# Performance work log

Hardware: AMD Instinct MI355X
Metric: run time of the kernel (lower is better)

## Reference

```python
import jax, jax.numpy as jnp
import numpy as np

D_MODEL = 1024
NUM_HEADS = 16
HEAD_DIM = D_MODEL // NUM_HEADS
B, S = 2, 2048


def setup_inputs() -> dict:
    key = jax.random.key(0)
    ks = jax.random.split(key, 8)
    scale = 1.0 / np.sqrt(D_MODEL)
    inp = {
        "query": jax.random.normal(ks[0], (B, S, D_MODEL), jnp.float32),
        "key": jax.random.normal(ks[1], (B, S, D_MODEL), jnp.float32),
        "value": jax.random.normal(ks[2], (B, S, D_MODEL), jnp.float32),
        # causal mask, broadcastable over batch and heads
        "mask": jnp.tril(jnp.ones((S, S), dtype=bool))[None, None, :, :],
        # torch nn.Linear weights: y = x @ W.T (+ b)
        "Wq": jax.random.normal(ks[3], (D_MODEL, D_MODEL), jnp.float32) * scale,
        "Wk": jax.random.normal(ks[4], (D_MODEL, D_MODEL), jnp.float32) * scale,
        "Wv": jax.random.normal(ks[5], (D_MODEL, D_MODEL), jnp.float32) * scale,
        "Wo": jax.random.normal(ks[6], (D_MODEL, D_MODEL), jnp.float32) * scale,
        "bo": jax.random.normal(ks[7], (D_MODEL,), jnp.float32) * scale,
    }
    return inp


def _split_heads(x):
    b, s, _ = x.shape
    return x.reshape(b, s, NUM_HEADS, HEAD_DIM).transpose(0, 2, 1, 3)  # [B,H,S,Dh]


def reference(query, key, value, mask, Wq, Wk, Wv, Wo, bo):
    q = _split_heads(query @ Wq.T)
    k = _split_heads(key @ Wk.T)
    v = _split_heads(value @ Wv.T)
    scores = jnp.einsum("bhqd,bhkd->bhqk", q, k) / jnp.sqrt(jnp.float32(HEAD_DIM))
    scores = jnp.where(mask, scores, jnp.float32(-jnp.inf))
    attn = jax.nn.softmax(scores, axis=-1)
    out = jnp.einsum("bhqk,bhkd->bhqd", attn, v)  # [B,H,S,Dh]
    out = out.transpose(0, 2, 1, 3).reshape(query.shape[0], q.shape[2], D_MODEL)
    return out @ Wo.T + bo
```

## Files before the change

kernel.cpp:

```cpp
#include <hip/hip_runtime.h>
#include <hip/hip_bf16.h>

#define DM   1024
#define NH   16
#define HD   64
#define SEQ  2048
#define BATCH 2
#define MTOT (BATCH*SEQ)

typedef unsigned short u16;
typedef __attribute__((ext_vector_type(8))) short bf16x8;
typedef __attribute__((ext_vector_type(4))) float f32x4;

__device__ __forceinline__ float bf2f(u16 h) {
  union { unsigned int i; float f; } u; u.i = ((unsigned int)h) << 16; return u.f;
}
__device__ __forceinline__ u16 f2bf(float f) {
  union { float f; unsigned int i; } u; u.f = f;
  unsigned int r = u.i + 0x7fffu + ((u.i >> 16) & 1u);
  return (u16)(r >> 16);
}

__global__ void detect_dtype(const u16* __restrict__ q, int* __restrict__ flag) {
  const int lane = threadIdx.x & 63;
  int cnt = 0;
  for (int i = 0; i < 8; i++) {
    int e = (q[i*64 + lane] >> 7) & 0xFF;
    unsigned long long m = __ballot(e >= 0x6E && e <= 0x8F);
    cnt += __popcll(m);
  }
  if (lane == 0) *flag = (cnt >= 400) ? 1 : 0;
}

__device__ __forceinline__ uint4 load8_bf16(const void* base, size_t elemOff, bool isf32) {
  if (!isf32) return *(const uint4*)((const u16*)base + elemOff);
  const float* f = (const float*)base + elemOff;
  f32x4 a = *(const f32x4*)f;
  f32x4 b = *(const f32x4*)(f + 4);
  union { u16 h[8]; uint4 v; } r;
  r.h[0]=f2bf(a[0]); r.h[1]=f2bf(a[1]); r.h[2]=f2bf(a[2]); r.h[3]=f2bf(a[3]);
  r.h[4]=f2bf(b[0]); r.h[5]=f2bf(b[1]); r.h[6]=f2bf(b[2]); r.h[7]=f2bf(b[3]);
  return r.v;
}

__global__ __launch_bounds__(256) void prep(
    const void* __restrict__ q, const void* __restrict__ k, const void* __restrict__ v,
    const void* __restrict__ wq, const void* __restrict__ wk, const void* __restrict__ wv,
    const void* __restrict__ wo, const void* __restrict__ bo,
    u16* __restrict__ Xq, u16* __restrict__ Xk, u16* __restrict__ Xv,
    u16* __restrict__ Wqb, u16* __restrict__ Wkb, u16* __restrict__ Wvb, u16* __restrict__ Wob,
    float* __restrict__ biasf, const int* __restrict__ dflag)
{
  const bool isf32 = (*dflag == 0);
  const int z = blockIdx.z;
  if (z == 7) {
    if (blockIdx.x == 0) {
      for (int i = threadIdx.x; i < DM; i += 256)
        biasf[i] = isf32 ? ((const float*)bo)[i] : bf2f(((const u16*)bo)[i]);
    }
    return;
  }
  const void* src; u16* dst; size_t n;
  switch (z) {
    case 0: src=q;  dst=Xq;  n=(size_t)MTOT*DM; break;
    case 1: src=k;  dst=Xk;  n=(size_t)MTOT*DM; break;
    case 2: src=v;  dst=Xv;  n=(size_t)MTOT*DM; break;
    case 3: src=wq; dst=Wqb; n=(size_t)DM*DM;   break;
    case 4: src=wk; dst=Wkb; n=(size_t)DM*DM;   break;
    case 5: src=wv; dst=Wvb; n=(size_t)DM*DM;   break;
    default: src=wo; dst=Wob; n=(size_t)DM*DM;  break;
  }
  const size_t stride = (size_t)gridDim.x * 256 * 8;
  for (size_t i = ((size_t)blockIdx.x * 256 + threadIdx.x) * 8; i < n; i += stride)
    *(uint4*)(dst + i) = load8_bf16(src, i, isf32);
}

__device__ __forceinline__ void gld16(const u16* g, u16* l) {
  __builtin_amdgcn_global_load_lds(
      (const __attribute__((address_space(1))) void*)g,
      (__attribute__((address_space(3))) void*)l, 16, 0, 0);
}

template<int MODE>
__global__ __launch_bounds__(256) void gemm128(
    const u16* __restrict__ X0, const u16* __restrict__ X1, const u16* __restrict__ X2,
    const u16* __restrict__ W0, const u16* __restrict__ W1, const u16* __restrict__ W2,
    const float* __restrict__ biasf,
    u16* __restrict__ F0, u16* __restrict__ F1, u16* __restrict__ F2,
    void* __restrict__ outP, const int* __restrict__ dflag)
{
  __shared__ u16 As[128*32];
  __shared__ u16 Bs[128*32];

  const u16* X; const u16* W; u16* outF = nullptr; int zz = 0;
  if (MODE == 0) {
    zz = blockIdx.z;
    X    = (zz==0) ? X0 : ((zz==1) ? X1 : X2);
    W    = (zz==0) ? W0 : ((zz==1) ? W1 : W2);
    outF = (zz==0) ? F0 : ((zz==1) ? F1 : F2);
  } else { X = X0; W = W0; }

  const int tid = threadIdx.x;
  const int wave = tid >> 6, lane = tid & 63, quad = lane >> 4, l16 = lane & 15;
  const int wr = wave >> 1, wc = wave & 1;
  const int m0 = blockIdx.y * 128, n0 = blockIdx.x * 128;

  const int sg = ((lane & 3) ^ ((lane >> 3) & 3)) * 8;
  const int rS = wave*32 + (lane >> 2);
  const u16* gA0 = X + (size_t)(m0 + rS)*DM + sg;
  const u16* gA1 = X + (size_t)(m0 + rS + 16)*DM + sg;
  const u16* gB0 = W + (size_t)(n0 + rS)*DM + sg;
  const u16* gB1 = W + (size_t)(n0 + rS + 16)*DM + sg;
  u16* lA0 = &As[wave*1024];
  u16* lA1 = &As[wave*1024 + 512];
  u16* lB0 = &Bs[wave*1024];
  u16* lB1 = &Bs[wave*1024 + 512];

  const int xslot8 = (quad ^ ((l16 >> 1) & 3)) * 8;

  f32x4 acc[4][4];
#pragma unroll
  for (int i = 0; i < 4; i++)
#pragma unroll
    for (int j = 0; j < 4; j++) { acc[i][j][0]=0.f; acc[i][j][1]=0.f; acc[i][j][2]=0.f; acc[i][j][3]=0.f; }

  for (int k0 = 0; k0 < DM; k0 += 32) {
    __syncthreads();
    gld16(gA0 + k0, lA0);
    gld16(gA1 + k0, lA1);
    gld16(gB0 + k0, lB0);
    gld16(gB1 + k0, lB1);
    __syncthreads();

    bf16x8 af[4], bfr[4];
#pragma unroll
    for (int fr = 0; fr < 4; fr++)
      af[fr] = *(const bf16x8*)&As[(wr*64 + fr*16 + l16)*32 + xslot8];
#pragma unroll
    for (int fc = 0; fc < 4; fc++)
      bfr[fc] = *(const bf16x8*)&Bs[(wc*64 + fc*16 + l16)*32 + xslot8];
#pragma unroll
    for (int fr = 0; fr < 4; fr++)
#pragma unroll
      for (int fc = 0; fc < 4; fc++)
        acc[fr][fc] = __builtin_amdgcn_mfma_f32_16x16x32_bf16(af[fr], bfr[fc], acc[fr][fc], 0, 0, 0);
  }

  const bool isf32 = (MODE == 1) && (*dflag == 0);
#pragma unroll
  for (int fr = 0; fr < 4; fr++) {
#pragma unroll
    for (int rr = 0; rr < 4; rr++) {
      const int m = m0 + wr*64 + fr*16 + quad*4 + rr;
#pragma unroll
      for (int fc = 0; fc < 4; fc++) {
        const int n = n0 + wc*64 + fc*16 + l16;
        float vv = acc[fr][fc][rr];
        if (MODE == 0) {
          const int b = m >> 11, s = m & (SEQ-1), h = n >> 6, d = n & (HD-1);
          if (zz == 2)
            outF[((size_t)(b*NH + h)*HD + d)*SEQ + s] = f2bf(vv);
          else
            outF[((size_t)(b*NH + h)*SEQ + s)*HD + d] = f2bf(vv);
        } else {
          vv += biasf[n];
          if (isf32) ((float*)outP)[(size_t)m*DM + n] = vv;
          else       ((u16*)outP)[(size_t)m*DM + n]   = f2bf(vv);
        }
      }
    }
  }
}

__global__ __launch_bounds__(256) void attn_mfma(
    const u16* __restrict__ Qb, const u16* __restrict__ Kb,
    const u16* __restrict__ Vtb, u16* __restrict__ attnO)
{
  __shared__ u16 Qs[64][72];
  __shared__ u16 Ks[64][72];
  __shared__ u16 Vs[64][72];
  __shared__ u16 Ps[4][16][72];

  const int bh = blockIdx.x;
  const int qt = blockIdx.y;
  const int b = bh >> 4, h = bh & 15;
  const int q0 = qt * 64;
  const u16* Qp = Qb  + (size_t)bh * SEQ * HD;
  const u16* Kp = Kb  + (size_t)bh * SEQ * HD;
  const u16* Vp = Vtb + (size_t)bh * HD * SEQ;

  const int tid  = threadIdx.x;
  const int wave = tid >> 6, lane = tid & 63, quad = lane >> 4, l16 = lane & 15;
  const int sr = tid >> 3, sc = (tid & 7) * 8;

  *(uint4*)&Qs[sr][sc]      = *(const uint4*)&Qp[(size_t)(q0 + sr)*HD + sc];
  *(uint4*)&Qs[sr + 32][sc] = *(const uint4*)&Qp[(size_t)(q0 + sr + 32)*HD + sc];

  const int qg = q0 + wave*16 + l16;
  f32x4 O[4];
#pragma unroll
  for (int u = 0; u < 4; u++) { O[u][0]=0.f; O[u][1]=0.f; O[u][2]=0.f; O[u][3]=0.f; }
  float mi = -__builtin_inff(), li = 0.f;

  for (int kt = 0; kt <= qt; kt++) {
    __syncthreads();
    *(uint4*)&Ks[sr][sc]      = *(const uint4*)&Kp[(size_t)(kt*64 + sr)*HD + sc];
    *(uint4*)&Ks[sr + 32][sc] = *(const uint4*)&Kp[(size_t)(kt*64 + sr + 32)*HD + sc];
    *(uint4*)&Vs[sr][sc]      = *(const uint4*)&Vp[(size_t)sr*SEQ + kt*64 + sc];
    *(uint4*)&Vs[sr + 32][sc] = *(const uint4*)&Vp[(size_t)(sr + 32)*SEQ + kt*64 + sc];
    __syncthreads();

    f32x4 st[4];
#pragma unroll
    for (int t = 0; t < 4; t++) { st[t][0]=0.f; st[t][1]=0.f; st[t][2]=0.f; st[t][3]=0.f; }
#pragma unroll
    for (int s = 0; s < 2; s++) {
      bf16x8 bq = *(const bf16x8*)&Qs[wave*16 + l16][s*32 + quad*8];
#pragma unroll
      for (int t = 0; t < 4; t++) {
        bf16x8 ak = *(const bf16x8*)&Ks[t*16 + l16][s*32 + quad*8];
        st[t] = __builtin_amdgcn_mfma_f32_16x16x32_bf16(ak, bq, st[t], 0, 0, 0);
      }
    }

    float v[4][4];
#pragma unroll
    for (int t = 0; t < 4; t++)
#pragma unroll
      for (int r = 0; r < 4; r++) v[t][r] = st[t][r] * 0.125f;
    if (kt == qt) {
#pragma unroll
      for (int t = 0; t < 4; t++)
#pragma unroll
        for (int r = 0; r < 4; r++)
          if (kt*64 + t*16 + quad*4 + r > qg) v[t][r] = -__builtin_inff();
    }
    float mx = v[0][0];
#pragma unroll
    for (int t = 0; t < 4; t++)
#pragma unroll
      for (int r = 0; r < 4; r++) mx = fmaxf(mx, v[t][r]);
    mx = fmaxf(mx, __shfl_xor(mx, 16));
    mx = fmaxf(mx, __shfl_xor(mx, 32));
    const float nm = fmaxf(mi, mx);
    const float al = __expf(mi - nm);
    float ps = 0.f;
#pragma unroll
    for (int t = 0; t < 4; t++) {
      union { u16 h[4]; uint2 u2; } pk;
#pragma unroll
      for (int r = 0; r < 4; r++) {
        const float p = __expf(v[t][r] - nm);
        ps += p;
        pk.h[r] = f2bf(p);
      }
      *(uint2*)&Ps[wave][l16][t*16 + quad*4] = pk.u2;
    }
    ps += __shfl_xor(ps, 16);
    ps += __shfl_xor(ps, 32);
    li = li * al + ps;
    mi = nm;
#pragma unroll
    for (int u = 0; u < 4; u++) {
      O[u][0] *= al; O[u][1] *= al; O[u][2] *= al; O[u][3] *= al;
    }
    __syncthreads();

#pragma unroll
    for (int s = 0; s < 2; s++) {
      bf16x8 bp = *(const bf16x8*)&Ps[wave][l16][s*32 + quad*8];
#pragma unroll
      for (int u = 0; u < 4; u++) {
        bf16x8 av = *(const bf16x8*)&Vs[u*16 + l16][s*32 + quad*8];
        O[u] = __builtin_amdgcn_mfma_f32_16x16x32_bf16(av, bp, O[u], 0, 0, 0);
      }
    }
  }

  const float inv = 1.0f / li;
  u16* op = attnO + (size_t)(b*SEQ + qg)*DM + h*HD;
#pragma unroll
  for (int u = 0; u < 4; u++) {
    union { u16 h[4]; uint2 u2; } pk;
#pragma unroll
    for (int r = 0; r < 4; r++) pk.h[r] = f2bf(O[u][r] * inv);
    *(uint2*)&op[u*16 + quad*4] = pk.u2;
  }
}

extern "C" void kernel_launch(void* const* d_in, const int* in_sizes, int n_in,
                              void* d_out, int out_size, void* d_ws, size_t ws_size,
                              hipStream_t stream) {
  const void* q  = d_in[0];
  const void* k  = d_in[1];
  const void* v  = d_in[2];
  const void* wq = d_in[4];
  const void* wk = d_in[5];
  const void* wv = d_in[6];
  const void* wo = d_in[7];
  const void* bo = d_in[8];

  const size_t TX = (size_t)MTOT*DM;
  const size_t TW = (size_t)DM*DM;
  u16* ws  = (u16*)d_ws;
  u16* Xq  = ws;
  u16* Xk  = ws + TX;
  u16* Xv  = ws + 2*TX;
  u16* Wqb = ws + 3*TX;
  u16* Wkb = Wqb + TW;
  u16* Wvb = Wqb + 2*TW;
  u16* Wob = Wqb + 3*TW;
  u16* Qw  = ws + 3*TX + 4*TW;
  u16* Kw  = Qw + TX;
  u16* Vt  = Qw + 2*TX;
  u16* aO  = Xq;
  float* biasf = (float*)(Qw + 3*TX);
  int*   fl    = (int*)(biasf + DM);

  dim3 blk(256);
  detect_dtype<<<1, 64, 0, stream>>>((const u16*)q, fl);
  prep<<<dim3(512, 1, 8), blk, 0, stream>>>(q, k, v, wq, wk, wv, wo, bo,
      Xq, Xk, Xv, Wqb, Wkb, Wvb, Wob, biasf, fl);
  gemm128<0><<<dim3(DM/128, MTOT/128, 3), blk, 0, stream>>>(
      Xq, Xk, Xv, Wqb, Wkb, Wvb, nullptr, Qw, Kw, Vt, nullptr, fl);
  attn_mfma<<<dim3(BATCH*NH, SEQ/64), blk, 0, stream>>>(Qw, Kw, Vt, aO);
  gemm128<1><<<dim3(DM/128, MTOT/128, 1), blk, 0, stream>>>(
      aO, nullptr, nullptr, Wob, nullptr, nullptr, biasf, nullptr, nullptr, nullptr, d_out, fl);
}
```

Measured before the change: 254.6 us.

## Balance causal attention with paired query tiles, split-K halves and a merge kernel

The attention kernel now gives each block two query tiles, pr and 31-pr, so every block does about the same amount of causal work. The key range of each tile is also split into two halves along a new grid dimension z. Each half writes an unnormalized bf16 partial output plus its running max and sum, and a new attn_merge kernel combines the two halves and normalizes the result. The softmax uses exp2 with the scale folded into one constant, and bf16 packing uses a cheaper rounding helper. The aim is to remove the tail imbalance of causal tiles, at the cost of an extra launch and extra global traffic for the partials, plus small precision changes from bf16 partials and the new rounding.

```diff
diff --git a/kernel.cpp b/kernel.cpp
--- a/kernel.cpp
+++ b/kernel.cpp
@@ -19,6 +19,10 @@
   union { float f; unsigned int i; } u; u.f = f;
   unsigned int r = u.i + 0x7fffu + ((u.i >> 16) & 1u);
   return (u16)(r >> 16);
+}
+__device__ __forceinline__ unsigned int pk2(float lo, float hi) {
+  union { float f; unsigned int u; } a, b; a.f = lo; b.f = hi;
+  return ((a.u + 0x8000u) >> 16) | ((b.u + 0x8000u) & 0xFFFF0000u);
 }
 
 __global__ void detect_dtype(const u16* __restrict__ q, int* __restrict__ flag) {
@@ -174,7 +178,8 @@
 
 __global__ __launch_bounds__(256) void attn_mfma(
     const u16* __restrict__ Qb, const u16* __restrict__ Kb,
-    const u16* __restrict__ Vtb, u16* __restrict__ attnO)
+    const u16* __restrict__ Vtb,
+    u16* __restrict__ Opart, float* __restrict__ mlpart)
 {
   __shared__ u16 Qs[64][72];
   __shared__ u16 Ks[64][72];
@@ -182,9 +187,7 @@
   __shared__ u16 Ps[4][16][72];
 
   const int bh = blockIdx.x;
-  const int qt = blockIdx.y;
-  const int b = bh >> 4, h = bh & 15;
-  const int q0 = qt * 64;
+  const int pr = blockIdx.y, z = blockIdx.z;
   const u16* Qp = Qb  + (size_t)bh * SEQ * HD;
   const u16* Kp = Kb  + (size_t)bh * SEQ * HD;
   const u16* Vp = Vtb + (size_t)bh * HD * SEQ;
@@ -192,99 +195,144 @@
   const int tid  = threadIdx.x;
   const int wave = tid >> 6, lane = tid & 63, quad = lane >> 4, l16 = lane & 15;
   const int sr = tid >> 3, sc = (tid & 7) * 8;
-
-  *(uint4*)&Qs[sr][sc]      = *(const uint4*)&Qp[(size_t)(q0 + sr)*HD + sc];
-  *(uint4*)&Qs[sr + 32][sc] = *(const uint4*)&Qp[(size_t)(q0 + sr + 32)*HD + sc];
-
-  const int qg = q0 + wave*16 + l16;
-  f32x4 O[4];
-#pragma unroll
-  for (int u = 0; u < 4; u++) { O[u][0]=0.f; O[u][1]=0.f; O[u][2]=0.f; O[u][3]=0.f; }
-  float mi = -__builtin_inff(), li = 0.f;
-
-  for (int kt = 0; kt <= qt; kt++) {
+  const float SC2 = 0.1803368801f;
+
+  for (int ph = 0; ph < 2; ph++) {
+    const int qt = ph ? (31 - pr) : pr;
+    const int n = qt + 1, half = (n + 1) >> 1;
+    const int klo = z ? half : 0, khi = z ? n : half;
+    const int q0 = qt * 64;
+
     __syncthreads();
-    *(uint4*)&Ks[sr][sc]      = *(const uint4*)&Kp[(size_t)(kt*64 + sr)*HD + sc];
-    *(uint4*)&Ks[sr + 32][sc] = *(const uint4*)&Kp[(size_t)(kt*64 + sr + 32)*HD + sc];
-    *(uint4*)&Vs[sr][sc]      = *(const uint4*)&Vp[(size_t)sr*SEQ + kt*64 + sc];
-    *(uint4*)&Vs[sr + 32][sc] = *(const uint4*)&Vp[(size_t)(sr + 32)*SEQ + kt*64 + sc];
-    __syncthreads();
-
-    f32x4 st[4];
-#pragma unroll
-    for (int t = 0; t < 4; t++) { st[t][0]=0.f; st[t][1]=0.f; st[t][2]=0.f; st[t][3]=0.f; }
-#pragma unroll
-    for (int s = 0; s < 2; s++) {
-      bf16x8 bq = *(const bf16x8*)&Qs[wave*16 + l16][s*32 + quad*8];
+    *(uint4*)&Qs[sr][sc]      = *(const uint4*)&Qp[(size_t)(q0 + sr)*HD + sc];
+    *(uint4*)&Qs[sr + 32][sc] = *(const uint4*)&Qp[(size_t)(q0 + sr + 32)*HD + sc];
+
+    const int ql = wave*16 + l16;
+    const int qg = q0 + ql;
+    f32x4 O[4];
+#pragma unroll
+    for (int u = 0; u < 4; u++) { O[u][0]=0.f; O[u][1]=0.f; O[u][2]=0.f; O[u][3]=0.f; }
+    float mi = -__builtin_inff(), li = 0.f;
+
+    for (int kt = klo; kt < khi; kt++) {
+      __syncthreads();
+      *(uint4*)&Ks[sr][sc]      = *(const uint4*)&Kp[(size_t)(kt*64 + sr)*HD + sc];
+      *(uint4*)&Ks[sr + 32][sc] = *(const uint4*)&Kp[(size_t)(kt*64 + sr + 32)*HD + sc];
+      *(uint4*)&Vs[sr][sc]      = *(const uint4*)&Vp[(size_t)sr*SEQ + kt*64 + sc];
+      *(uint4*)&Vs[sr + 32][sc] = *(const uint4*)&Vp[(size_t)(sr + 32)*SEQ + kt*64 + sc];
+      __syncthreads();
+
+      f32x4 st[4];
+#pragma unroll
+      for (int t = 0; t < 4; t++) { st[t][0]=0.f; st[t][1]=0.f; st[t][2]=0.f; st[t][3]=0.f; }
+#pragma unroll
+      for (int s = 0; s < 2; s++) {
+        bf16x8 bq = *(const bf16x8*)&Qs[ql][s*32 + quad*8];
+#pragma unroll
+        for (int t = 0; t < 4; t++) {
+          bf16x8 ak = *(const bf16x8*)&Ks[t*16 + l16][s*32 + quad*8];
+          st[t] = __builtin_amdgcn_mfma_f32_16x16x32_bf16(ak, bq, st[t], 0, 0, 0);
+        }
+      }
+
+      float v[4][4];
+#pragma unroll
+      for (int t = 0; t < 4; t++)
+#pragma unroll
+        for (int r = 0; r < 4; r++) v[t][r] = st[t][r] * SC2;
+      if (kt == qt) {
+#pragma unroll
+        for (int t = 0; t < 4; t++)
+#pragma unroll
+          for (int r = 0; r < 4; r++)
+            if (kt*64 + t*16 + quad*4 + r > qg) v[t][r] = -__builtin_inff();
+      }
+      float mx = v[0][0];
+#pragma unroll
+      for (int t = 0; t < 4; t++)
+#pragma unroll
+        for (int r = 0; r < 4; r++) mx = fmaxf(mx, v[t][r]);
+      mx = fmaxf(mx, __shfl_xor(mx, 16));
+      mx = fmaxf(mx, __shfl_xor(mx, 32));
+      const float nm = fmaxf(mi, mx);
+      const float al = exp2f(mi - nm);
+      float ps = 0.f;
 #pragma unroll
       for (int t = 0; t < 4; t++) {
-        bf16x8 ak = *(const bf16x8*)&Ks[t*16 + l16][s*32 + quad*8];
-        st[t] = __builtin_amdgcn_mfma_f32_16x16x32_bf16(ak, bq, st[t], 0, 0, 0);
-      }
-    }
-
-    float v[4][4];
-#pragma unroll
-    for (int t = 0; t < 4; t++)
-#pragma unroll
-      for (int r = 0; r < 4; r++) v[t][r] = st[t][r] * 0.125f;
-    if (kt == qt) {
-#pragma unroll
-      for (int t = 0; t < 4; t++)
-#pragma unroll
-        for (int r = 0; r < 4; r++)
-          if (kt*64 + t*16 + quad*4 + r > qg) v[t][r] = -__builtin_inff();
-    }
-    float mx = v[0][0];
-#pragma unroll
-    for (int t = 0; t < 4; t++)
-#pragma unroll
-      for (int r = 0; r < 4; r++) mx = fmaxf(mx, v[t][r]);
-    mx = fmaxf(mx, __shfl_xor(mx, 16));
-    mx = fmaxf(mx, __shfl_xor(mx, 32));
-    const float nm = fmaxf(mi, mx);
-    const float al = __expf(mi - nm);
-    float ps = 0.f;
-#pragma unroll
-    for (int t = 0; t < 4; t++) {
-      union { u16 h[4]; uint2 u2; } pk;
-#pragma unroll
-      for (int r = 0; r < 4; r++) {
-        const float p = __expf(v[t][r] - nm);
-        ps += p;
-        pk.h[r] = f2bf(p);
-      }
-      *(uint2*)&Ps[wave][l16][t*16 + quad*4] = pk.u2;
-    }
-    ps += __shfl_xor(ps, 16);
-    ps += __shfl_xor(ps, 32);
-    li = li * al + ps;
-    mi = nm;
+        float p0 = exp2f(v[t][0] - nm), p1 = exp2f(v[t][1] - nm);
+        float p2 = exp2f(v[t][2] - nm), p3 = exp2f(v[t][3] - nm);
+        ps += (p0 + p1) + (p2 + p3);
+        uint2 u2; u2.x = pk2(p0, p1); u2.y = pk2(p2, p3);
+        *(uint2*)&Ps[wave][l16][t*16 + quad*4] = u2;
+      }
+      ps += __shfl_xor(ps, 16);
+      ps += __shfl_xor(ps, 32);
+      li = li * al + ps;
+      mi = nm;
+#pragma unroll
+      for (int u = 0; u < 4; u++) {
+        O[u][0] *= al; O[u][1] *= al; O[u][2] *= al; O[u][3] *= al;
+      }
+      __syncthreads();
+
+#pragma unroll
+      for (int s = 0; s < 2; s++) {
+        bf16x8 bp = *(const bf16x8*)&Ps[wave][l16][s*32 + quad*8];
+#pragma unroll
+        for (int u = 0; u < 4; u++) {
+          bf16x8 av = *(const bf16x8*)&Vs[u*16 + l16][s*32 + quad*8];
+          O[u] = __builtin_amdgcn_mfma_f32_16x16x32_bf16(av, bp, O[u], 0, 0, 0);
+        }
+      }
+    }
+
+    const int pi = (bh*32 + qt)*2 + z;
+    u16* op = Opart + (size_t)pi*4096 + ql*64;
 #pragma unroll
     for (int u = 0; u < 4; u++) {
-      O[u][0] *= al; O[u][1] *= al; O[u][2] *= al; O[u][3] *= al;
-    }
-    __syncthreads();
-
-#pragma unroll
-    for (int s = 0; s < 2; s++) {
-      bf16x8 bp = *(const bf16x8*)&Ps[wave][l16][s*32 + quad*8];
-#pragma unroll
-      for (int u = 0; u < 4; u++) {
-        bf16x8 av = *(const bf16x8*)&Vs[u*16 + l16][s*32 + quad*8];
-        O[u] = __builtin_amdgcn_mfma_f32_16x16x32_bf16(av, bp, O[u], 0, 0, 0);
-      }
-    }
-  }
-
-  const float inv = 1.0f / li;
-  u16* op = attnO + (size_t)(b*SEQ + qg)*DM + h*HD;
-#pragma unroll
-  for (int u = 0; u < 4; u++) {
-    union { u16 h[4]; uint2 u2; } pk;
-#pragma unroll
-    for (int r = 0; r < 4; r++) pk.h[r] = f2bf(O[u][r] * inv);
-    *(uint2*)&op[u*16 + quad*4] = pk.u2;
+      uint2 u2; u2.x = pk2(O[u][0], O[u][1]); u2.y = pk2(O[u][2], O[u][3]);
+      *(uint2*)&op[u*16 + quad*4] = u2;
+    }
+    if (quad == 0) {
+      float2 ml2; ml2.x = mi; ml2.y = li;
+      *(float2*)&mlpart[(size_t)pi*128 + ql*2] = ml2;
+    }
+  }
+}
+
+__global__ __launch_bounds__(64) void attn_merge(
+    const u16* __restrict__ Opart, const float* __restrict__ mlpart,
+    u16* __restrict__ aO)
+{
+  const int g = blockIdx.x;
+  const int bh = g & 31, qt = g >> 5;
+  const int b = bh >> 4, h = bh & 15;
+  const int t = threadIdx.x;
+  const int pi0 = (bh*32 + qt)*2, pi1 = pi0 + 1;
+
+  const float2 ml0 = *(const float2*)&mlpart[(size_t)pi0*128 + t*2];
+  const float2 ml1 = *(const float2*)&mlpart[(size_t)pi1*128 + t*2];
+  const float M = fmaxf(ml0.x, ml1.x);
+  float w0 = exp2f(ml0.x - M), w1 = exp2f(ml1.x - M);
+  const float inv = 1.0f / (w0*ml0.y + w1*ml1.y);
+  w0 *= inv; w1 *= inv;
+
+  const u16* o0 = Opart + (size_t)pi0*4096 + t*64;
+  const u16* o1 = Opart + (size_t)pi1*4096 + t*64;
+  u16* out = aO + (size_t)(b*SEQ + qt*64 + t)*DM + h*HD;
+#pragma unroll
+  for (int d0 = 0; d0 < 64; d0 += 8) {
+    union { uint4 v; u16 h[8]; } a, c; union { uint4 v; u16 h[8]; } bb;
+    a.v  = *(const uint4*)&o0[d0];
+    bb.v = *(const uint4*)&o1[d0];
+#pragma unroll
+    for (int j = 0; j < 8; j += 2) {
+      float x0 = w0*bf2f(a.h[j])   + w1*bf2f(bb.h[j]);
+      float x1 = w0*bf2f(a.h[j+1]) + w1*bf2f(bb.h[j+1]);
+      unsigned int pk = pk2(x0, x1);
+      c.h[j] = (u16)(pk & 0xFFFF); c.h[j+1] = (u16)(pk >> 16);
+    }
+    *(uint4*)&out[d0] = c.v;
   }
 }
 
@@ -313,9 +361,11 @@
   u16* Qw  = ws + 3*TX + 4*TW;
   u16* Kw  = Qw + TX;
   u16* Vt  = Qw + 2*TX;
-  u16* aO  = Xq;
-  float* biasf = (float*)(Qw + 3*TX);
-  int*   fl    = (int*)(biasf + DM);
+  u16*   Opart  = Xk;
+  float* mlpart = (float*)Wqb;
+  u16*   aO     = Xq;
+  float* biasf  = (float*)(Qw + 3*TX);
+  int*   fl     = (int*)(biasf + DM);
 
   dim3 blk(256);
   detect_dtype<<<1, 64, 0, stream>>>((const u16*)q, fl);
@@ -323,7 +373,8 @@
       Xq, Xk, Xv, Wqb, Wkb, Wvb, Wob, biasf, fl);
   gemm128<0><<<dim3(DM/128, MTOT/128, 3), blk, 0, stream>>>(
       Xq, Xk, Xv, Wqb, Wkb, Wvb, nullptr, Qw, Kw, Vt, nullptr, fl);
-  attn_mfma<<<dim3(BATCH*NH, SEQ/64), blk, 0, stream>>>(Qw, Kw, Vt, aO);
+  attn_mfma<<<dim3(BATCH*NH, 16, 2), blk, 0, stream>>>(Qw, Kw, Vt, Opart, mlpart);
+  attn_merge<<<dim3(32*32), dim3(64), 0, stream>>>(Opart, mlpart, aO);
   gemm128<1><<<dim3(DM/128, MTOT/128, 1), blk, 0, stream>>>(
       aO, nullptr, nullptr, Wob, nullptr, nullptr, biasf, nullptr, nullptr, nullptr, d_out, fl);
 }
```

Result: no change. 255.0 us (+0.1%).
